# Kernel optimization log

Hardware: AMD Instinct MI355X
Metric: run time of the kernel (lower is better)

## Reference

```python
import jax, jax.numpy as jnp
import numpy as np

N_NODES = 100000
N_EDGES = 1600000
N_GRAPHS = 2048
HID = 64
IN_F = 14
N_CLS = 2
EPS = 1e-5


def _gcn_conv(x, row, col, w_edge, W, b, n_nodes):
    # PyG GCNConv with add_self_loops=True, normalize=True.
    xw = x @ W  # [N, out]
    # degree on target nodes, self-loop contributes weight 1
    deg = jnp.zeros((n_nodes,), x.dtype).at[col].add(w_edge) + 1.0
    dinv = deg ** -0.5
    norm = dinv[row] * w_edge * dinv[col]  # [E]
    out = jnp.zeros_like(xw).at[col].add(norm[:, None] * xw[row])
    out = out + (dinv * dinv)[:, None] * xw  # self-loop term
    return out + b


def _bn_relu(x, gamma, beta):
    mean = jnp.mean(x, axis=0)
    var = jnp.var(x, axis=0)  # biased, as PyTorch BN training normalization
    y = gamma * (x - mean) * jax.lax.rsqrt(var + EPS) + beta
    return jax.nn.relu(y)


def setup_inputs() -> dict:
    key = jax.random.key(0)
    ks = jax.random.split(key, 8)
    x = jax.random.normal(ks[0], (N_NODES, IN_F), dtype=jnp.float32)
    edge_index = jax.random.randint(ks[1], (2, N_EDGES), 0, N_NODES, dtype=jnp.int64)
    batch = jnp.sort(jax.random.randint(ks[2], (N_NODES,), 0, N_GRAPHS, dtype=jnp.int64))
    edge_weight = jnp.ones((N_EDGES,), dtype=jnp.float32)
    def lin(k, fi, fo):
        s = 1.0 / np.sqrt(fi)
        kw, kb = jax.random.split(k)
        return (jax.random.uniform(kw, (fi, fo), jnp.float32, -s, s),
                jax.random.uniform(kb, (fo,), jnp.float32, -s, s))
    W1, b1 = lin(ks[3], IN_F, HID)
    W2, b2 = lin(ks[4], HID, HID)
    W3, b3 = lin(ks[5], HID, HID)
    fcW, fcb = lin(ks[6], HID, N_CLS)
    g = jnp.ones((HID,), jnp.float32)
    z = jnp.zeros((HID,), jnp.float32)
    return {
        "x": x, "edge_index": edge_index, "batch": batch, "edge_weight": edge_weight,
        "W1": W1, "b1": b1, "W2": W2, "b2": b2, "W3": W3, "b3": b3,
        "g1": g, "bt1": z, "g2": g, "bt2": z, "g3": g, "bt3": z,
        "fcW": fcW, "fcb": fcb,
    }


def reference(x, edge_index, batch, edge_weight, W1, b1, W2, b2, W3, b3,
              g1, bt1, g2, bt2, g3, bt3, fcW, fcb):
    row, col = edge_index[0], edge_index[1]
    n = x.shape[0]
    h = _bn_relu(_gcn_conv(x, row, col, edge_weight, W1, b1, n), g1, bt1)
    h = _bn_relu(_gcn_conv(h, row, col, edge_weight, W2, b2, n), g2, bt2)
    h = _bn_relu(_gcn_conv(h, row, col, edge_weight, W3, b3, n), g3, bt3)
    node_embs = h  # dropout p=0 is identity
    graph_emb = jax.ops.segment_sum(node_embs, batch, num_segments=N_GRAPHS)
    out = graph_emb @ fcW + fcb
    return (out, node_embs, graph_emb)
```

## Files before the change

### kernel.cpp

```cpp
#include <hip/hip_runtime.h>

#define N_NODES 100000
#define N_EDGES 1600000
#define N_GRAPHS 2048
#define HID 64
#define IN_F 14
#define N_CLS 2
#define EPS 1e-5f

#define BSHIFT 9
#define NBUCK 196
#define ABLOCKS 256
#define CHUNK (N_EDGES / ABLOCKS)

#define NBLK2 128
#define NCHUNK2 ((N_NODES + NBLK2 - 1) / NBLK2)

typedef _Float16 half_t;
typedef _Float16 half8 __attribute__((ext_vector_type(8)));
typedef float f32x4 __attribute__((ext_vector_type(4)));

#define GSTRIDE ((size_t)N_NODES * 16)


__global__ __launch_bounds__(256) void histA_kernel(const int* __restrict__ col,
                                                    int* __restrict__ histG) {
    __shared__ int hl[NBUCK];
    for (int i = threadIdx.x; i < NBUCK; i += 256) hl[i] = 0;
    __syncthreads();
    int e0 = blockIdx.x * CHUNK;
    for (int e = e0 + threadIdx.x; e < e0 + CHUNK; e += 256)
        atomicAdd(&hl[col[e] >> BSHIFT], 1);
    __syncthreads();
    for (int i = threadIdx.x; i < NBUCK; i += 256)
        histG[i * ABLOCKS + blockIdx.x] = hl[i];
}

__global__ __launch_bounds__(256) void scanS1_kernel(const int* __restrict__ histG,
                                                     int* __restrict__ bsumA) {
    __shared__ int ls[256];
    ls[threadIdx.x] = histG[blockIdx.x * 256 + threadIdx.x];
    __syncthreads();
    for (int off = 128; off > 0; off >>= 1) {
        if (threadIdx.x < off) ls[threadIdx.x] += ls[threadIdx.x + off];
        __syncthreads();
    }
    if (threadIdx.x == 0) bsumA[blockIdx.x] = ls[0];
}

__global__ __launch_bounds__(512) void topscan_kernel(int* __restrict__ bsum, int nb) {
    __shared__ int ls[512];
    int t = threadIdx.x;
    int v = (t < nb) ? bsum[t] : 0;
    ls[t] = v;
    __syncthreads();
    for (int off = 1; off < 512; off <<= 1) {
        int x = ls[t];
        if (t >= off) x += ls[t - off];
        __syncthreads();
        ls[t] = x;
        __syncthreads();
    }
    if (t < nb) bsum[t] = ls[t] - v;
}

__global__ __launch_bounds__(256) void scanS3_kernel(int* __restrict__ histG,
                                                     const int* __restrict__ bsumA,
                                                     int* __restrict__ ptr) {
    __shared__ int ls[256];
    int idx = blockIdx.x * 256 + threadIdx.x;
    int v = histG[idx];
    ls[threadIdx.x] = v;
    __syncthreads();
    for (int off = 1; off < 256; off <<= 1) {
        int x = ls[threadIdx.x];
        if (threadIdx.x >= off) x += ls[threadIdx.x - off];
        __syncthreads();
        ls[threadIdx.x] = x;
        __syncthreads();
    }
    histG[idx] = ls[threadIdx.x] - v + bsumA[blockIdx.x];
    if (blockIdx.x == 0 && threadIdx.x == 0) ptr[N_NODES] = N_EDGES;
}

__global__ __launch_bounds__(256) void scatterA_kernel(const int* __restrict__ row,
                                                       const int* __restrict__ col,
                                                       const float* __restrict__ w,
                                                       const int* __restrict__ histG,
                                                       int2* __restrict__ EA) {
    __shared__ int cur[NBUCK];
    for (int i = threadIdx.x; i < NBUCK; i += 256)
        cur[i] = histG[i * ABLOCKS + blockIdx.x];
    __syncthreads();
    int e0 = blockIdx.x * CHUNK;
    for (int e = e0 + threadIdx.x; e < e0 + CHUNK; e += 256) {
        int c = col[e];
        int r = row[e];
        int fx = (int)__float2uint_rn(w[e] * 8192.0f);
        int pos = atomicAdd(&cur[c >> BSHIFT], 1);
        EA[pos] = make_int2(r, (fx << 17) | c);
    }
}

__global__ __launch_bounds__(256) void bucket_kernel(const int2* __restrict__ EA,
                                                     const int* __restrict__ bsumA,
                                                     int2* __restrict__ EB,
                                                     int* __restrict__ ptr,
                                                     float* __restrict__ dinv) {
    __shared__ int hist[512], wsum[512], cur[512];
    int b = blockIdx.x;
    int beg = bsumA[b];
    int end = (b == NBUCK - 1) ? N_EDGES : bsumA[b + 1];
    int i0 = threadIdx.x, i1 = threadIdx.x + 256;
    hist[i0] = 0; hist[i1] = 0;
    wsum[i0] = 0; wsum[i1] = 0;
    __syncthreads();
    for (int e = beg + threadIdx.x; e < end; e += 256) {
        int2 ed = EA[e];
        int c9 = ed.y & 511;
        atomicAdd(&hist[c9], 1);
        atomicAdd(&wsum[c9], (int)((unsigned int)ed.y >> 17));
    }
    __syncthreads();
    int cnt0 = hist[i0], cnt1 = hist[i1];
    for (int off = 1; off < 512; off <<= 1) {
        int v0 = hist[i0], v1 = hist[i1];
        int a0 = (i0 >= off) ? hist[i0 - off] : 0;
        int a1 = (i1 >= off) ? hist[i1 - off] : 0;
        __syncthreads();
        hist[i0] = v0 + a0;
        hist[i1] = v1 + a1;
        __syncthreads();
    }
    int excl0 = hist[i0] - cnt0, excl1 = hist[i1] - cnt1;
    cur[i0] = beg + excl0;
    cur[i1] = beg + excl1;
    int col0 = (b << BSHIFT) + i0, col1 = (b << BSHIFT) + i1;
    if (col0 < N_NODES) {
        ptr[col0] = beg + excl0;
        dinv[col0] = rsqrtf(1.0f + (float)wsum[i0] * (1.0f / 8192.0f));
    }
    if (col1 < N_NODES) {
        ptr[col1] = beg + excl1;
        dinv[col1] = rsqrtf(1.0f + (float)wsum[i1] * (1.0f / 8192.0f));
    }
    __syncthreads();
    for (int e = beg + threadIdx.x; e < end; e += 256) {
        int2 ed = EA[e];
        int pos = atomicAdd(&cur[ed.y & 511], 1);
        EB[pos] = ed;
    }
}


__global__ __launch_bounds__(256) void histD_kernel(const int* __restrict__ ptr,
                                                    int* __restrict__ histD) {
    __shared__ int hl[2048];
    for (int i = threadIdx.x; i < 2048; i += 256) hl[i] = 0;
    __syncthreads();
    int n0 = blockIdx.x * NCHUNK2;
    int n1 = n0 + NCHUNK2; if (n1 > N_NODES) n1 = N_NODES;
    for (int n = n0 + threadIdx.x; n < n1; n += 256) {
        int d = ptr[n + 1] - ptr[n];
        if (d > 255) d = 255;
        atomicAdd(&hl[((threadIdx.x & 7) << 8) + d], 1);
    }
    __syncthreads();
    int s = 0;
#pragma unroll
    for (int c = 0; c < 8; c++) s += hl[(c << 8) + threadIdx.x];
    histD[threadIdx.x * NBLK2 + blockIdx.x] = s;
}

__global__ __launch_bounds__(128) void scanD1_kernel(const int* __restrict__ histD,
                                                     int* __restrict__ rowTot) {
    __shared__ int ls[128];
    ls[threadIdx.x] = histD[blockIdx.x * NBLK2 + threadIdx.x];
    __syncthreads();
    for (int off = 64; off > 0; off >>= 1) {
        if (threadIdx.x < off) ls[threadIdx.x] += ls[threadIdx.x + off];
        __syncthreads();
    }
    if (threadIdx.x == 0) rowTot[blockIdx.x] = ls[0];
}

__global__ __launch_bounds__(256) void topscanD_kernel(const int* __restrict__ rowTot,
                                                       int* __restrict__ nodeExcl,
                                                       int* __restrict__ edgeExcl,
                                                       int* __restrict__ ptrS) {
    __shared__ int a[256], b[256];
    int t = threadIdx.x;
    int cnt = rowTot[t];
    int ec = cnt * t;
    a[t] = cnt; b[t] = ec;
    __syncthreads();
    for (int off = 1; off < 256; off <<= 1) {
        int va = a[t], vb = b[t];
        if (t >= off) { va += a[t - off]; vb += b[t - off]; }
        __syncthreads();
        a[t] = va; b[t] = vb;
        __syncthreads();
    }
    nodeExcl[t] = a[t] - cnt;
    edgeExcl[t] = b[t] - ec;
    if (t == 0) ptrS[N_NODES] = N_EDGES;
}

__global__ __launch_bounds__(128) void scanD3_kernel(int* __restrict__ histD,
                                                     const int* __restrict__ nodeExcl) {
    __shared__ int ls[128];
    int idx = blockIdx.x * NBLK2 + threadIdx.x;
    int v = histD[idx];
    ls[threadIdx.x] = v;
    __syncthreads();
    for (int off = 1; off < 128; off <<= 1) {
        int x = ls[threadIdx.x];
        if (threadIdx.x >= off) x += ls[threadIdx.x - off];
        __syncthreads();
        ls[threadIdx.x] = x;
        __syncthreads();
    }
    histD[idx] = ls[threadIdx.x] - v + nodeExcl[blockIdx.x];
}

__global__ __launch_bounds__(256) void scatterD_kernel(const int* __restrict__ ptr,
                                                       const int* __restrict__ histD,
                                                       const int* __restrict__ nodeExcl,
                                                       const int* __restrict__ edgeExcl,
                                                       int* __restrict__ perm,
                                                       int* __restrict__ ptrS,
                                                       int* __restrict__ newbase) {
    __shared__ int cur[256];
    cur[threadIdx.x] = histD[threadIdx.x * NBLK2 + blockIdx.x];
    __syncthreads();
    int n0 = blockIdx.x * NCHUNK2;
    int n1 = n0 + NCHUNK2; if (n1 > N_NODES) n1 = N_NODES;
    for (int n = n0 + threadIdx.x; n < n1; n += 256) {
        int d = ptr[n + 1] - ptr[n];
        if (d > 255) d = 255;
        int pos = atomicAdd(&cur[d], 1);
        int ebase = edgeExcl[d] + (pos - nodeExcl[d]) * d;
        perm[pos] = n;
        ptrS[pos] = ebase;
        newbase[n] = ebase;
    }
}

__global__ __launch_bounds__(256) void finalize_kernel(const int2* __restrict__ EB,
                                                       const float* __restrict__ dinv,
                                                       const int* __restrict__ ptr,
                                                       const int* __restrict__ newbase,
                                                       unsigned int* __restrict__ edges, int E) {
    int stride = gridDim.x * blockDim.x;
    for (int e = blockIdx.x * blockDim.x + threadIdx.x; e < E; e += stride) {
        int2 ed = EB[e];
        int c = ed.y & 0x1ffff;
        float w = (float)((unsigned int)ed.y >> 17) * (1.0f / 8192.0f);
        float nrm = dinv[ed.x] * w * dinv[c];
        unsigned int nb = __float_as_uint(nrm);
        unsigned int n15 = (nb + 0x8000u) >> 16;
        if (n15 > 0x7fffu) n15 = 0x7fffu;
        int newpos = newbase[c] + (e - ptr[c]);
        edges[newpos] = ((unsigned int)ed.x << 15) | n15;
    }
}


template <int K>
__global__ __launch_bounds__(256) void gemm_kernel(const float* __restrict__ h,
                                                   const float* __restrict__ W,
                                                   half_t* __restrict__ xw, int n_nodes) {
    int f = threadIdx.x & 63;
    float wcol[K];
#pragma unroll
    for (int k = 0; k < K; k++) wcol[k] = W[k * HID + f];
    half_t* xg = xw + (size_t)(f >> 4) * GSTRIDE + (f & 15);
    int wave = (blockIdx.x * blockDim.x + threadIdx.x) >> 6;
    int nwaves = (gridDim.x * blockDim.x) >> 6;
    for (int n = wave; n < n_nodes; n += nwaves) {
        const float* hr = h + (size_t)n * K;
        float acc = 0.f;
#pragma unroll
        for (int k = 0; k < K; k++) acc += hr[k] * wcol[k];
        xg[(size_t)n * 16] = (half_t)acc;
    }
}

__global__ __launch_bounds__(256) void gemm_bn_mfma_kernel(const half_t* __restrict__ h,
                                                           const float* __restrict__ W,
                                                           const float* __restrict__ stats,
                                                           const float* __restrict__ gamma,
                                                           const float* __restrict__ beta,
                                                           half_t* __restrict__ xw, int n_nodes) {
    __shared__ float sc_s[HID], sh_s[HID];
    if (threadIdx.x < 64) {
        float mean = stats[threadIdx.x] * (1.0f / N_NODES);
        float var = stats[64 + threadIdx.x] * (1.0f / N_NODES) - mean * mean;
        float sc = gamma[threadIdx.x] * rsqrtf(var + EPS);
        sc_s[threadIdx.x] = sc;
        sh_s[threadIdx.x] = beta[threadIdx.x] - mean * sc;
    }
    __syncthreads();
    int lane = threadIdx.x & 63;
    int col16 = lane & 15;
    int quad = lane >> 4;

    float scA[2][8], shA[2][8];
#pragma unroll
    for (int kh = 0; kh < 2; kh++)
#pragma unroll
        for (int j = 0; j < 8; j++) {
            int k = kh * 32 + quad * 8 + j;
            scA[kh][j] = sc_s[k];
            shA[kh][j] = sh_s[k];
        }

    half8 bfrag[4][2];
#pragma unroll
    for (int t = 0; t < 4; t++)
#pragma unroll
        for (int kh = 0; kh < 2; kh++)
#pragma unroll
            for (int j = 0; j < 8; j++) {
                int k = kh * 32 + quad * 8 + j;
                bfrag[t][kh][j] = (half_t)W[k * HID + t * 16 + col16];
            }

    int wave = (blockIdx.x * blockDim.x + threadIdx.x) >> 6;
    int nwaves = (gridDim.x * blockDim.x) >> 6;
    int ntiles = n_nodes >> 4;
    for (int tIdx = wave; tIdx < ntiles; tIdx += nwaves) {
        int n0 = tIdx << 4;
        half8 afrag[2];
#pragma unroll
        for (int kh = 0; kh < 2; kh++) {
            int k0 = kh * 32 + quad * 8;
            const half_t* hp = h + (size_t)(k0 >> 4) * GSTRIDE
                                 + (size_t)(n0 + col16) * 16 + (k0 & 15);
            half8 raw = *(const half8*)hp;
#pragma unroll
            for (int j = 0; j < 8; j++) {
                float v = (float)raw[j] * scA[kh][j] + shA[kh][j];
                afrag[kh][j] = (half_t)fmaxf(v, 0.f);
            }
        }
        f32x4 acc[4];
#pragma unroll
        for (int t = 0; t < 4; t++) {
            f32x4 z = {0.f, 0.f, 0.f, 0.f};
            acc[t] = __builtin_amdgcn_mfma_f32_16x16x32_f16(afrag[0], bfrag[t][0], z, 0, 0, 0);
            acc[t] = __builtin_amdgcn_mfma_f32_16x16x32_f16(afrag[1], bfrag[t][1], acc[t], 0, 0, 0);
        }
#pragma unroll
        for (int t = 0; t < 4; t++) {
            half_t* xg = xw + (size_t)t * GSTRIDE;
#pragma unroll
            for (int r = 0; r < 4; r++) {
                int rowi = n0 + quad * 4 + r;
                xg[(size_t)rowi * 16 + col16] = (half_t)acc[t][r];
            }
        }
    }
}

template <bool LAST>
__global__ __launch_bounds__(256) void gather_stats_kernel(const int* __restrict__ ptrS,
                                                           const int* __restrict__ perm,
                                                           const unsigned int* __restrict__ edges,
                                                           const half_t* __restrict__ xw,
                                                           const float* __restrict__ dinv,
                                                           const float* __restrict__ b,
                                                           half_t* __restrict__ hp,
                                                           float* __restrict__ hf,
                                                           float* __restrict__ stats,
                                                           int n_nodes) {
    int g = (blockIdx.x & 7) >> 1;
    int grank = ((blockIdx.x >> 3) << 1) | (blockIdx.x & 1);
    int lane16 = threadIdx.x & 15;
    int quadLocal = threadIdx.x >> 4;
    int quadId = grank * 16 + quadLocal;
    int nquads = (gridDim.x >> 2) * 16;

    const half_t* xg = xw + (size_t)g * GSTRIDE;
    const char* xgb = (const char*)xg + lane16 * 2;
    half_t* hpg = hp + (size_t)g * GSTRIDE;
    int f = g * 16 + lane16;
    float bf = b[f];
    int base = ((threadIdx.x & 63) >> 4) * 16;

    float s = 0.f, s2 = 0.f;
    for (int i = quadId; i < n_nodes; i += nquads) {
        int node = perm[i];
        int beg = ptrS[i];
        int c = ptrS[i + 1] - beg;
        float a0 = 0.f, a1 = 0.f, a2 = 0.f, a3 = 0.f;
        for (int j0 = 0; j0 < c; j0 += 16) {
            int m = c - j0;
            if (m > 16) m = 16;
            int ev = 0;
            if (lane16 < m) ev = (int)edges[beg + j0 + lane16];
            int j = 0;
            for (; j + 4 <= m; j += 4) {
                unsigned int u0 = (unsigned int)__shfl(ev, base + j);
                unsigned int u1 = (unsigned int)__shfl(ev, base + j + 1);
                unsigned int u2 = (unsigned int)__shfl(ev, base + j + 2);
                unsigned int u3 = (unsigned int)__shfl(ev, base + j + 3);
                float w0 = __uint_as_float((u0 & 0x7fffu) << 16);
                float w1 = __uint_as_float((u1 & 0x7fffu) << 16);
                float w2 = __uint_as_float((u2 & 0x7fffu) << 16);
                float w3 = __uint_as_float((u3 & 0x7fffu) << 16);
                float x0 = (float)*(const half_t*)(xgb + ((size_t)(u0 >> 15) << 5));
                float x1 = (float)*(const half_t*)(xgb + ((size_t)(u1 >> 15) << 5));
                float x2 = (float)*(const half_t*)(xgb + ((size_t)(u2 >> 15) << 5));
                float x3 = (float)*(const half_t*)(xgb + ((size_t)(u3 >> 15) << 5));
                a0 += w0 * x0; a1 += w1 * x1; a2 += w2 * x2; a3 += w3 * x3;
            }
            if (j < m) {
                unsigned int u = (unsigned int)__shfl(ev, base + j);
                a1 += __uint_as_float((u & 0x7fffu) << 16) *
                      (float)*(const half_t*)(xgb + ((size_t)(u >> 15) << 5));
            }
            if (j + 1 < m) {
                unsigned int u = (unsigned int)__shfl(ev, base + j + 1);
                a2 += __uint_as_float((u & 0x7fffu) << 16) *
                      (float)*(const half_t*)(xgb + ((size_t)(u >> 15) << 5));
            }
            if (j + 2 < m) {
                unsigned int u = (unsigned int)__shfl(ev, base + j + 2);
                a3 += __uint_as_float((u & 0x7fffu) << 16) *
                      (float)*(const half_t*)(xgb + ((size_t)(u >> 15) << 5));
            }
        }
        float di = dinv[node];
        float v = ((a0 + a1) + (a2 + a3))
                  + di * di * (float)xg[(size_t)node * 16 + lane16] + bf;
        if (LAST)
            hf[(size_t)node * HID + f] = v;
        else
            hpg[(size_t)node * 16 + lane16] = (half_t)v;
        s += v;
        s2 += v * v;
    }
    __shared__ float ls[256], ls2[256];
    ls[threadIdx.x] = s;
    ls2[threadIdx.x] = s2;
    __syncthreads();
    if (threadIdx.x < 16) {
        float a = 0.f, aa = 0.f;
#pragma unroll
        for (int k = 0; k < 16; k++) {
            a += ls[k * 16 + threadIdx.x];
            aa += ls2[k * 16 + threadIdx.x];
        }
        atomicAdd(&stats[g * 16 + threadIdx.x], a);
        atomicAdd(&stats[64 + g * 16 + threadIdx.x], aa);
    }
}

__global__ __launch_bounds__(256) void bn_relu_seg_kernel(float* __restrict__ h,
                                                          const float* __restrict__ stats,
                                                          const float* __restrict__ gamma,
                                                          const float* __restrict__ beta,
                                                          const int* __restrict__ batch,
                                                          float* __restrict__ gemb,
                                                          int n_nodes) {
    int g = blockIdx.x * blockDim.x + threadIdx.x;
    int f = g & 63;
    int wave = g >> 6;
    int nwaves = (gridDim.x * blockDim.x) >> 6;
    int chunk = (n_nodes + nwaves - 1) / nwaves;
    int n0 = wave * chunk;
    int n1 = n0 + chunk;
    if (n1 > n_nodes) n1 = n_nodes;
    if (n0 >= n_nodes) return;
    float mean = stats[f] * (1.0f / N_NODES);
    float var = stats[64 + f] * (1.0f / N_NODES) - mean * mean;
    float sc = gamma[f] * rsqrtf(var + EPS);
    float sh = beta[f] - mean * sc;
    int curg = batch[n0];
    float racc = 0.f;
    for (int n = n0; n < n1; n++) {
        int bg = batch[n];
        if (bg != curg) {
            atomicAdd(&gemb[(size_t)curg * HID + f], racc);
            racc = 0.f;
            curg = bg;
        }
        size_t idx = (size_t)n * HID + f;
        float v = h[idx] * sc + sh;
        v = fmaxf(v, 0.f);
        h[idx] = v;
        racc += v;
    }
    atomicAdd(&gemb[(size_t)curg * HID + f], racc);
}

__global__ __launch_bounds__(256) void final_kernel(const float* __restrict__ gemb,
                                                    const float* __restrict__ fcW,
                                                    const float* __restrict__ fcb,
                                                    float* __restrict__ out) {
    int g = blockIdx.x * blockDim.x + threadIdx.x;
    if (g >= N_GRAPHS * N_CLS) return;
    int gr = g >> 1, c = g & 1;
    float acc = fcb[c];
#pragma unroll
    for (int k = 0; k < HID; k++) acc += gemb[gr * HID + k] * fcW[k * N_CLS + c];
    out[g] = acc;
}


extern "C" void kernel_launch(void* const* d_in, const int* in_sizes, int n_in,
                              void* d_out, int out_size, void* d_ws, size_t ws_size,
                              hipStream_t stream) {
    const float* x    = (const float*)d_in[0];
    const int*   ei   = (const int*)d_in[1];
    const int*   batch= (const int*)d_in[2];
    const float* ew   = (const float*)d_in[3];
    const float* W1   = (const float*)d_in[4];
    const float* b1   = (const float*)d_in[5];
    const float* W2   = (const float*)d_in[6];
    const float* b2   = (const float*)d_in[7];
    const float* W3   = (const float*)d_in[8];
    const float* b3   = (const float*)d_in[9];
    const float* g1   = (const float*)d_in[10];
    const float* bt1  = (const float*)d_in[11];
    const float* g2   = (const float*)d_in[12];
    const float* bt2  = (const float*)d_in[13];
    const float* g3   = (const float*)d_in[14];
    const float* bt3  = (const float*)d_in[15];
    const float* fcW  = (const float*)d_in[16];
    const float* fcb  = (const float*)d_in[17];

    const int* row = ei;
    const int* col = ei + N_EDGES;

    float* out_head  = (float*)d_out;
    float* node_embs = out_head + N_GRAPHS * N_CLS;
    float* gemb      = node_embs + (size_t)N_NODES * HID;

    char* bse = (char*)d_ws;
    half_t* xwh = (half_t*)bse;
    int2*   EB  = (int2*)bse;
    char* r1 = bse + (size_t)N_NODES * HID * 2;
    int2*   EA  = (int2*)r1;
    half_t* hpl = (half_t*)r1;
    char* r2 = r1 + (size_t)N_NODES * HID * 2;
    unsigned int* edges = (unsigned int*)r2;
    char* r3 = r2 + (size_t)N_EDGES * 4;
    float* dinv  = (float*)r3;
    float* stats = dinv + N_NODES;
    int*   ptr   = (int*)(stats + 128);
    int*   histG = ptr + N_NODES + 1;
    int*   bsumA = histG + NBUCK * ABLOCKS;
    int*   histD = bsumA + NBUCK + 4;
    int*   rowTot = histD + 256 * NBLK2;
    int*   nodeExcl = rowTot + 256;
    int*   edgeExcl = nodeExcl + 256;
    int*   perm   = edgeExcl + 256;
    int*   newbase= perm + N_NODES;
    int*   ptrS   = newbase + N_NODES;

    const int B   = 256;
    const int gGS = 1024;
    const int gGA = 2048;

    histA_kernel<<<ABLOCKS, B, 0, stream>>>(col, histG);
    scanS1_kernel<<<NBUCK, B, 0, stream>>>(histG, bsumA);
    topscan_kernel<<<1, 512, 0, stream>>>(bsumA, NBUCK);
    scanS3_kernel<<<NBUCK, B, 0, stream>>>(histG, bsumA, ptr);
    scatterA_kernel<<<ABLOCKS, B, 0, stream>>>(row, col, ew, histG, EA);
    bucket_kernel<<<NBUCK, B, 0, stream>>>(EA, bsumA, EB, ptr, dinv);

    histD_kernel<<<NBLK2, B, 0, stream>>>(ptr, histD);
    scanD1_kernel<<<256, 128, 0, stream>>>(histD, rowTot);
    topscanD_kernel<<<1, 256, 0, stream>>>(rowTot, nodeExcl, edgeExcl, ptrS);
    scanD3_kernel<<<256, 128, 0, stream>>>(histD, nodeExcl);
    scatterD_kernel<<<NBLK2, B, 0, stream>>>(ptr, histD, nodeExcl, edgeExcl,
                                             perm, ptrS, newbase);
    finalize_kernel<<<gGS, B, 0, stream>>>(EB, dinv, ptr, newbase, edges, N_EDGES);

    float* h3 = node_embs;

    gemm_kernel<IN_F><<<gGS, B, 0, stream>>>(x, W1, xwh, N_NODES);
    hipMemsetAsync(stats, 0, 128 * sizeof(float), stream);
    gather_stats_kernel<false><<<gGA, B, 0, stream>>>(ptrS, perm, edges, xwh, dinv,
                                                      b1, hpl, h3, stats, N_NODES);

    gemm_bn_mfma_kernel<<<gGS, B, 0, stream>>>(hpl, W2, stats, g1, bt1, xwh, N_NODES);
    hipMemsetAsync(stats, 0, 128 * sizeof(float), stream);
    gather_stats_kernel<false><<<gGA, B, 0, stream>>>(ptrS, perm, edges, xwh, dinv,
                                                      b2, hpl, h3, stats, N_NODES);

    gemm_bn_mfma_kernel<<<gGS, B, 0, stream>>>(hpl, W3, stats, g2, bt2, xwh, N_NODES);
    hipMemsetAsync(stats, 0, 128 * sizeof(float), stream);
    gather_stats_kernel<true><<<gGA, B, 0, stream>>>(ptrS, perm, edges, xwh, dinv,
                                                     b3, hpl, h3, stats, N_NODES);

    hipMemsetAsync(gemb, 0, (size_t)N_GRAPHS * HID * sizeof(float), stream);
    bn_relu_seg_kernel<<<gGS, B, 0, stream>>>(h3, stats, g3, bt3, batch, gemb, N_NODES);

    final_kernel<<<(N_GRAPHS * N_CLS + B - 1) / B, B, 0, stream>>>(gemb, fcW, fcb, out_head);
}
```

Measured before the change: 418.4 us.

## Pad per-node edge lists to multiples of eight and load edges as vectors

Each node's CSR edge segment is now padded to a multiple of eight entries and the packed edge buffer is zeroed, so padding entries carry zero weight and index node 0. The gather loop reads edges directly with two 16-byte vector loads per eight neighbours and uses eight accumulators. This replaces the cross-lane shuffle broadcast and the remainder handling. The cost is a larger edge buffer, an extra memset of about 9.6 MB, and wasted gathers on padding slots.

```diff
diff --git a/kernel.cpp b/kernel.cpp
--- a/kernel.cpp
+++ b/kernel.cpp
@@ -2,6 +2,7 @@
 
 #define N_NODES 100000
 #define N_EDGES 1600000
+#define EMAX    2400000
 #define N_GRAPHS 2048
 #define HID 64
 #define IN_F 14
@@ -19,6 +20,7 @@
 typedef _Float16 half_t;
 typedef _Float16 half8 __attribute__((ext_vector_type(8)));
 typedef float f32x4 __attribute__((ext_vector_type(4)));
+typedef unsigned int uint4v __attribute__((ext_vector_type(4)));
 
 #define GSTRIDE ((size_t)N_NODES * 16)
 
@@ -191,7 +193,8 @@
     __shared__ int a[256], b[256];
     int t = threadIdx.x;
     int cnt = rowTot[t];
-    int ec = cnt * t;
+    int dpad = (t + 7) & ~7;
+    int ec = cnt * dpad;
     a[t] = cnt; b[t] = ec;
     __syncthreads();
     for (int off = 1; off < 256; off <<= 1) {
@@ -203,7 +206,7 @@
     }
     nodeExcl[t] = a[t] - cnt;
     edgeExcl[t] = b[t] - ec;
-    if (t == 0) ptrS[N_NODES] = N_EDGES;
+    if (t == 255) ptrS[N_NODES] = b[255];
 }
 
 __global__ __launch_bounds__(128) void scanD3_kernel(int* __restrict__ histD,
@@ -238,8 +241,9 @@
     for (int n = n0 + threadIdx.x; n < n1; n += 256) {
         int d = ptr[n + 1] - ptr[n];
         if (d > 255) d = 255;
+        int dpad = (d + 7) & ~7;
         int pos = atomicAdd(&cur[d], 1);
-        int ebase = edgeExcl[d] + (pos - nodeExcl[d]) * d;
+        int ebase = edgeExcl[d] + (pos - nodeExcl[d]) * dpad;
         perm[pos] = n;
         ptrS[pos] = ebase;
         newbase[n] = ebase;
@@ -386,53 +390,36 @@
     half_t* hpg = hp + (size_t)g * GSTRIDE;
     int f = g * 16 + lane16;
     float bf = b[f];
-    int base = ((threadIdx.x & 63) >> 4) * 16;
 
     float s = 0.f, s2 = 0.f;
     for (int i = quadId; i < n_nodes; i += nquads) {
         int node = perm[i];
         int beg = ptrS[i];
-        int c = ptrS[i + 1] - beg;
+        int endp = ptrS[i + 1];
         float a0 = 0.f, a1 = 0.f, a2 = 0.f, a3 = 0.f;
-        for (int j0 = 0; j0 < c; j0 += 16) {
-            int m = c - j0;
-            if (m > 16) m = 16;
-            int ev = 0;
-            if (lane16 < m) ev = (int)edges[beg + j0 + lane16];
-            int j = 0;
-            for (; j + 4 <= m; j += 4) {
-                unsigned int u0 = (unsigned int)__shfl(ev, base + j);
-                unsigned int u1 = (unsigned int)__shfl(ev, base + j + 1);
-                unsigned int u2 = (unsigned int)__shfl(ev, base + j + 2);
-                unsigned int u3 = (unsigned int)__shfl(ev, base + j + 3);
-                float w0 = __uint_as_float((u0 & 0x7fffu) << 16);
-                float w1 = __uint_as_float((u1 & 0x7fffu) << 16);
-                float w2 = __uint_as_float((u2 & 0x7fffu) << 16);
-                float w3 = __uint_as_float((u3 & 0x7fffu) << 16);
-                float x0 = (float)*(const half_t*)(xgb + ((size_t)(u0 >> 15) << 5));
-                float x1 = (float)*(const half_t*)(xgb + ((size_t)(u1 >> 15) << 5));
-                float x2 = (float)*(const half_t*)(xgb + ((size_t)(u2 >> 15) << 5));
-                float x3 = (float)*(const half_t*)(xgb + ((size_t)(u3 >> 15) << 5));
-                a0 += w0 * x0; a1 += w1 * x1; a2 += w2 * x2; a3 += w3 * x3;
-            }
-            if (j < m) {
-                unsigned int u = (unsigned int)__shfl(ev, base + j);
-                a1 += __uint_as_float((u & 0x7fffu) << 16) *
-                      (float)*(const half_t*)(xgb + ((size_t)(u >> 15) << 5));
-            }
-            if (j + 1 < m) {
-                unsigned int u = (unsigned int)__shfl(ev, base + j + 1);
-                a2 += __uint_as_float((u & 0x7fffu) << 16) *
-                      (float)*(const half_t*)(xgb + ((size_t)(u >> 15) << 5));
-            }
-            if (j + 2 < m) {
-                unsigned int u = (unsigned int)__shfl(ev, base + j + 2);
-                a3 += __uint_as_float((u & 0x7fffu) << 16) *
-                      (float)*(const half_t*)(xgb + ((size_t)(u >> 15) << 5));
-            }
+        float a4 = 0.f, a5 = 0.f, a6 = 0.f, a7 = 0.f;
+        for (int j = beg; j < endp; j += 8) {
+            uint4v p0 = *(const uint4v*)(edges + j);
+            uint4v p1 = *(const uint4v*)(edges + j + 4);
+            float x0 = (float)*(const half_t*)(xgb + ((size_t)(p0.x >> 15) << 5));
+            float x1 = (float)*(const half_t*)(xgb + ((size_t)(p0.y >> 15) << 5));
+            float x2 = (float)*(const half_t*)(xgb + ((size_t)(p0.z >> 15) << 5));
+            float x3 = (float)*(const half_t*)(xgb + ((size_t)(p0.w >> 15) << 5));
+            float x4 = (float)*(const half_t*)(xgb + ((size_t)(p1.x >> 15) << 5));
+            float x5 = (float)*(const half_t*)(xgb + ((size_t)(p1.y >> 15) << 5));
+            float x6 = (float)*(const half_t*)(xgb + ((size_t)(p1.z >> 15) << 5));
+            float x7 = (float)*(const half_t*)(xgb + ((size_t)(p1.w >> 15) << 5));
+            a0 += __uint_as_float((p0.x & 0x7fffu) << 16) * x0;
+            a1 += __uint_as_float((p0.y & 0x7fffu) << 16) * x1;
+            a2 += __uint_as_float((p0.z & 0x7fffu) << 16) * x2;
+            a3 += __uint_as_float((p0.w & 0x7fffu) << 16) * x3;
+            a4 += __uint_as_float((p1.x & 0x7fffu) << 16) * x4;
+            a5 += __uint_as_float((p1.y & 0x7fffu) << 16) * x5;
+            a6 += __uint_as_float((p1.z & 0x7fffu) << 16) * x6;
+            a7 += __uint_as_float((p1.w & 0x7fffu) << 16) * x7;
         }
         float di = dinv[node];
-        float v = ((a0 + a1) + (a2 + a3))
+        float v = (((a0 + a1) + (a2 + a3)) + ((a4 + a5) + (a6 + a7)))
                   + di * di * (float)xg[(size_t)node * 16 + lane16] + bf;
         if (LAST)
             hf[(size_t)node * HID + f] = v;
@@ -546,7 +533,7 @@
     half_t* hpl = (half_t*)r1;
     char* r2 = r1 + (size_t)N_NODES * HID * 2;
     unsigned int* edges = (unsigned int*)r2;
-    char* r3 = r2 + (size_t)N_EDGES * 4;
+    char* r3 = r2 + (size_t)EMAX * 4;
     float* dinv  = (float*)r3;
     float* stats = dinv + N_NODES;
     int*   ptr   = (int*)(stats + 128);
@@ -577,6 +564,7 @@
     scanD3_kernel<<<256, 128, 0, stream>>>(histD, nodeExcl);
     scatterD_kernel<<<NBLK2, B, 0, stream>>>(ptr, histD, nodeExcl, edgeExcl,
                                              perm, ptrS, newbase);
+    hipMemsetAsync(edges, 0, (size_t)EMAX * 4, stream);
     finalize_kernel<<<gGS, B, 0, stream>>>(EB, dinv, ptr, newbase, edges, N_EDGES);
 
     float* h3 = node_embs;
```

Result: slower. 427.8 us (+2.2%).
